# Optimization experiments

Hardware: AMD Instinct MI355X
Metric: run time of the kernel (lower is better)

## Reference

```python
import jax, jax.numpy as jnp
import numpy as np

B, T, N, C, H, K, L, E = 8, 16, 512, 64, 64, 3, 2, 16384


def setup_inputs() -> dict:
    key = jax.random.key(0)
    ks = jax.random.split(key, 8)
    x = jax.random.normal(ks[0], (B, T, N, C), jnp.float32)
    edge_index = jax.random.randint(ks[1], (2, E), 0, N, dtype=jnp.int64)
    edge_weight = jax.random.uniform(ks[2], (E,), jnp.float32)
    s = 0.05
    # per layer l, gate g in (z, r, h): K Chebyshev weight mats for x-conv and h-conv
    Wx = jax.random.normal(ks[3], (L, 3, K, C, H), jnp.float32) * s
    bx = jnp.zeros((L, 3, H), jnp.float32)
    Wh = jax.random.normal(ks[4], (L, 3, K, H, H), jnp.float32) * s
    bh = jnp.zeros((L, 3, H), jnp.float32)
    W1 = jax.random.normal(ks[5], (2 * H, H), jnp.float32) * s
    b1 = jnp.zeros((H,), jnp.float32)
    W2 = jax.random.normal(ks[6], (H, 1), jnp.float32) * s
    b2 = jnp.zeros((1,), jnp.float32)
    return dict(x=x, edge_weight=edge_weight, Wx=Wx, bx=bx, Wh=Wh, bh=bh,
                W1=W1, b1=b1, W2=W2, b2=b2, edge_index=edge_index)


def _cheb(t, W, b, src, dst, norm_w):
    # ChebConv with sym norm, lambda_max=2: L_hat = -D^{-1/2} A D^{-1/2} (zero diag)
    # t: [B, N, Cin], W: [K, Cin, H], b: [H]
    def Lx(u):
        msg = u[:, src, :] * norm_w[None, :, None]  # gather + scale per edge
        return jnp.zeros_like(u).at[:, dst, :].add(msg)  # scatter-add to targets
    out = jnp.einsum('bnc,ch->bnh', t, W[0])
    Tprev, Tcur = t, Lx(t)
    out = out + jnp.einsum('bnc,ch->bnh', Tcur, W[1])
    for k in range(2, W.shape[0]):
        Tnext = 2.0 * Lx(Tcur) - Tprev
        out = out + jnp.einsum('bnc,ch->bnh', Tnext, W[k])
        Tprev, Tcur = Tcur, Tnext
    return out + b


def _gru_cell(x_t, h, Wx_l, bx_l, Wh_l, bh_l, src, dst, norm_w):
    z = jax.nn.sigmoid(_cheb(x_t, Wx_l[0], bx_l[0], src, dst, norm_w)
                       + _cheb(h, Wh_l[0], bh_l[0], src, dst, norm_w))
    r = jax.nn.sigmoid(_cheb(x_t, Wx_l[1], bx_l[1], src, dst, norm_w)
                       + _cheb(h, Wh_l[1], bh_l[1], src, dst, norm_w))
    h_tilde = jnp.tanh(_cheb(x_t, Wx_l[2], bx_l[2], src, dst, norm_w)
                       + _cheb(h * r, Wh_l[2], bh_l[2], src, dst, norm_w))
    return z * h + (1.0 - z) * h_tilde


def reference(x, edge_weight, Wx, bx, Wh, bh, W1, b1, W2, b2, edge_index):
    n = x.shape[2]
    src, dst = edge_index[0], edge_index[1]
    deg = jnp.zeros((n,), x.dtype).at[src].add(edge_weight)
    dinv = jnp.where(deg > 0, jax.lax.rsqrt(jnp.maximum(deg, 1e-12)), 0.0)
    norm_w = -edge_weight * dinv[src] * dinv[dst]

    def step(h, x_t):
        for l in range(Wx.shape[0]):  # note: original passes the SAME x_t to every layer
            h = _gru_cell(x_t, h, Wx[l], bx[l], Wh[l], bh[l], src, dst, norm_w)
        return h, None

    h0 = jnp.zeros((x.shape[0], n, Wh.shape[-1]), x.dtype)
    h, _ = jax.lax.scan(step, h0, jnp.moveaxis(x, 1, 0))  # dropout is identity (eval)

    # all-pairs link predictor: cat(src_emb, tgt_emb) @ W1 split to avoid 2H concat
    hh = W1.shape[1]
    s_proj = h @ W1[:hh]   # [B, N, H]
    t_proj = h @ W1[hh:]   # [B, N, H]
    hid = jax.nn.relu(s_proj[:, :, None, :] + t_proj[:, None, :, :] + b1)  # [B,N,N,H]
    logits = jnp.einsum('bsth,ho->bsto', hid, W2)[..., 0] + b2[0]  # [B, N, N]
    return logits
```

## Files before the change

kernel.cpp:

```cpp
#include <hip/hip_runtime.h>

typedef unsigned short ushort;
typedef unsigned long long u64;
typedef __attribute__((ext_vector_type(8))) short short8;
typedef __attribute__((ext_vector_type(4))) float f32x4;

constexpr int Bn = 8, Tn = 16, Nn = 512, Cn = 64, Hn = 64, En = 16384, Ln = 2;
constexpr int NC = Nn * Cn;
constexpr int MROWS = Bn * Nn;

constexpr size_t OFF_DEG  = 0;
constexpr size_t OFF_DINV = 512;
constexpr size_t OFF_L1D  = 1024;
constexpr size_t OFF_L2D  = OFF_L1D + 262144;
constexpr size_t OFF_WZR  = OFF_L2D + 262144;
constexpr size_t OFF_WHT  = OFF_WZR + 2*384*128;
constexpr size_t OFF_BZR  = OFF_WHT + 2*384*64;
constexpr size_t OFF_BHT  = OFF_BZR + 256;
constexpr size_t OFF_W1C  = OFF_BHT + 128;
constexpr size_t OFF_T1X  = OFF_W1C + 8192;
constexpr size_t OFF_T2X  = OFF_T1X + (size_t)Bn*Tn*NC;
constexpr size_t OFF_H    = OFF_T2X + (size_t)Bn*Tn*NC;
constexpr size_t OFF_Z    = OFF_H   + (size_t)Bn*NC;
constexpr size_t OFF_HR   = OFF_Z   + (size_t)Bn*NC;
constexpr size_t OFF_SP   = OFF_HR  + (size_t)Bn*NC;
constexpr size_t OFF_TP   = OFF_SP  + (size_t)MROWS*Hn;
constexpr size_t OFF_LFH  = OFF_TP  + (size_t)MROWS*Hn;
constexpr size_t OFF_LFL  = OFF_LFH + 262144;
constexpr size_t OFF_HTH  = OFF_LFL + 262144;
constexpr size_t OFF_HTL  = OFF_HTH + 131072;
constexpr size_t OFF_HRTH = OFF_HTL + 131072;
constexpr size_t OFF_HRTL = OFF_HRTH + 131072;
constexpr size_t OFF_BAR  = OFF_HRTL + 131072;
constexpr size_t OFF_END  = OFF_BAR + 4096;

__device__ __forceinline__ ushort f2bf(float f) {
    unsigned u = __float_as_uint(f);
    u = u + 0x7FFF + ((u >> 16) & 1);
    return (ushort)(u >> 16);
}
__device__ __forceinline__ float bf2f(ushort h) {
    return __uint_as_float(((unsigned)h) << 16);
}
__device__ __forceinline__ int fragaddr(int m, int k) {
    return ((k >> 5) << 9) + (((k >> 3) & 3) << 7) + (m << 3) + (k & 7);
}

#define MFMA16(a, b, c) __builtin_amdgcn_mfma_f32_16x16x32_bf16((a), (b), (c), 0, 0, 0)

__global__ void k_deg(const float* __restrict__ w, const int* __restrict__ src,
                      float* __restrict__ deg) {
    int e = blockIdx.x * 256 + threadIdx.x;
    if (e < En) atomicAdd(&deg[src[e]], w[e]);
}

__global__ void k_dinv(const float* __restrict__ deg, float* __restrict__ dinv) {
    int n = blockIdx.x * 256 + threadIdx.x;
    if (n < Nn) {
        float d = deg[n];
        dinv[n] = d > 0.f ? rsqrtf(fmaxf(d, 1e-12f)) : 0.f;
    }
}

__global__ void k_nwdense(const float* __restrict__ w, const int* __restrict__ src,
                          const int* __restrict__ dst, const float* __restrict__ dinv,
                          float* __restrict__ L1d) {
    int e = blockIdx.x * 256 + threadIdx.x;
    if (e < En) {
        int s = src[e], d = dst[e];
        float nw = -w[e] * dinv[s] * dinv[d];
        atomicAdd(&L1d[d * Nn + s], nw);
    }
}

__global__ __launch_bounds__(1024) void k_l2(const float* __restrict__ A,
                                             float* __restrict__ C) {
    __shared__ float As[64][33];
    __shared__ float Bs[32][65];
    int t = threadIdx.x;
    int i0 = (blockIdx.x >> 3) * 64;
    int j0 = (blockIdx.x & 7) * 64;
    int tx = t & 31, ty = t >> 5;
    float acc[2][2] = {};
    int ar = t >> 4, ac = (t & 15) * 2;
    int br = t >> 5, bc = (t & 31) * 2;
    for (int kc = 0; kc < 512; kc += 32) {
        float2 a2 = *(const float2*)&A[(size_t)(i0 + ar) * 512 + kc + ac];
        float2 b2 = *(const float2*)&A[(size_t)(kc + br) * 512 + j0 + bc];
        As[ar][ac] = a2.x; As[ar][ac + 1] = a2.y;
        Bs[br][bc] = b2.x; Bs[br][bc + 1] = b2.y;
        __syncthreads();
#pragma unroll 8
        for (int kk = 0; kk < 32; kk++) {
            float a0 = As[ty * 2][kk], a1 = As[ty * 2 + 1][kk];
            float b0 = Bs[kk][tx * 2], b1 = Bs[kk][tx * 2 + 1];
            acc[0][0] += a0 * b0; acc[0][1] += a0 * b1;
            acc[1][0] += a1 * b0; acc[1][1] += a1 * b1;
        }
        __syncthreads();
    }
#pragma unroll
    for (int r = 0; r < 2; r++)
#pragma unroll
        for (int c = 0; c < 2; c++) {
            int i = i0 + ty * 2 + r, j = j0 + tx * 2 + c;
            C[(size_t)i * 512 + j] = 2.f * acc[r][c] - (i == j ? 1.f : 0.f);
        }
}

__global__ void k_lfrag(const float* __restrict__ L1, const float* __restrict__ L2,
                        ushort* __restrict__ AfH, ushort* __restrict__ AfL) {
    int idx = blockIdx.x * 256 + threadIdx.x;
    int j = idx & 7;
    int lane = (idx >> 3) & 63;
    int kc = (idx >> 9) & 15;
    int rb = (idx >> 13) & 31;
    int mat = idx >> 18;
    int row = rb * 16 + (lane & 15);
    int k = kc * 32 + (lane >> 4) * 8 + j;
    float v = (mat ? L2 : L1)[(size_t)row * 512 + k];
    ushort hi = f2bf(v);
    AfH[idx] = hi;
    AfL[idx] = f2bf(v - bf2f(hi));
}

__global__ void k_wfrag(const float* __restrict__ WzrC, const float* __restrict__ WhC,
                        ushort* __restrict__ WzFH, ushort* __restrict__ WzFL,
                        ushort* __restrict__ WhFH, ushort* __restrict__ WhFL) {
    int idx = blockIdx.x * 256 + threadIdx.x;
    if (idx < 98304) {
        int l = idx / 49152, off = idx % 49152;
        int tile = off >> 9, r = off & 511;
        int lane = r >> 3, j = r & 7;
        int ct = tile / 12, kc = tile % 12;
        int k = kc * 32 + (lane >> 4) * 8 + j;
        int n = ct * 16 + (lane & 15);
        float v = WzrC[(size_t)l * 49152 + k * 128 + n];
        ushort hi = f2bf(v);
        WzFH[idx] = hi;
        WzFL[idx] = f2bf(v - bf2f(hi));
    } else if (idx < 147456) {
        int t2 = idx - 98304;
        int l = t2 / 24576, off = t2 % 24576;
        int tile = off >> 9, r = off & 511;
        int lane = r >> 3, j = r & 7;
        int ct = tile / 12, kc = tile % 12;
        int k = kc * 32 + (lane >> 4) * 8 + j;
        int n = ct * 16 + (lane & 15);
        float v = WhC[(size_t)l * 24576 + k * 64 + n];
        ushort hi = f2bf(v);
        WhFH[t2] = hi;
        WhFL[t2] = f2bf(v - bf2f(hi));
    }
}

__global__ __launch_bounds__(256) void k_lxm(
        const ushort* __restrict__ AfH, const ushort* __restrict__ AfL,
        const float* __restrict__ in, float* __restrict__ o1, float* __restrict__ o2) {
    __shared__ ushort Bh[2][2176];
    __shared__ ushort Bl[2][2176];
    int slice = blockIdx.x >> 3;
    int rg = blockIdx.x & 7;
    const float* xs = in + (size_t)slice * NC;
    int tid = threadIdx.x;
    int lane = tid & 63, wav = tid >> 6;
    int quad = lane >> 4, l15 = lane & 15;
    int sn = tid & 63, skq = tid >> 6;
    int rt = rg * 4 + wav;
    size_t abA = ((size_t)rt * 16) * 512 + lane * 8;
    size_t abB = ((size_t)(32 + rt) * 16) * 512 + lane * 8;
    f32x4 accA[4], accB[4];
#pragma unroll
    for (int n = 0; n < 4; n++) {
        accA[n] = (f32x4){0.f, 0.f, 0.f, 0.f};
        accB[n] = (f32x4){0.f, 0.f, 0.f, 0.f};
    }
    {
        short8 hi8, lo8;
#pragma unroll
        for (int i = 0; i < 8; i++) {
            float v = xs[(size_t)(skq * 8 + i) * 64 + sn];
            ushort hv = f2bf(v);
            hi8[i] = (short)hv;
            lo8[i] = (short)f2bf(v - bf2f(hv));
        }
        *(short8*)&Bh[0][sn * 34 + skq * 8] = hi8;
        *(short8*)&Bl[0][sn * 34 + skq * 8] = lo8;
    }
    __syncthreads();
#pragma unroll
    for (int kc = 0; kc < 16; kc++) {
        const int cur = kc & 1;
        float sv[8];
        if (kc < 15) {
#pragma unroll
            for (int i = 0; i < 8; i++)
                sv[i] = xs[(size_t)((kc + 1) * 32 + skq * 8 + i) * 64 + sn];
        }
        size_t o = (size_t)kc * 512;
        short8 lah = *(const short8*)&AfH[abA + o];
        short8 lal = *(const short8*)&AfL[abA + o];
        short8 lbh = *(const short8*)&AfH[abB + o];
        short8 lbl = *(const short8*)&AfL[abB + o];
#pragma unroll
        for (int nt = 0; nt < 4; nt++) {
            short8 xh = *(const short8*)&Bh[cur][(nt * 16 + l15) * 34 + quad * 8];
            short8 xl = *(const short8*)&Bl[cur][(nt * 16 + l15) * 34 + quad * 8];
            accA[nt] = MFMA16(lah, xh, accA[nt]);
            accA[nt] = MFMA16(lah, xl, accA[nt]);
            accA[nt] = MFMA16(lal, xh, accA[nt]);
            accB[nt] = MFMA16(lbh, xh, accB[nt]);
            accB[nt] = MFMA16(lbh, xl, accB[nt]);
            accB[nt] = MFMA16(lbl, xh, accB[nt]);
        }
        if (kc < 15) {
            short8 hi8, lo8;
#pragma unroll
            for (int i = 0; i < 8; i++) {
                ushort hv = f2bf(sv[i]);
                hi8[i] = (short)hv;
                lo8[i] = (short)f2bf(sv[i] - bf2f(hv));
            }
            *(short8*)&Bh[cur ^ 1][sn * 34 + skq * 8] = hi8;
            *(short8*)&Bl[cur ^ 1][sn * 34 + skq * 8] = lo8;
        }
        __syncthreads();
    }
    float* os1 = o1 + (size_t)slice * NC;
    float* os2 = o2 + (size_t)slice * NC;
#pragma unroll
    for (int nt = 0; nt < 4; nt++)
#pragma unroll
        for (int reg = 0; reg < 4; reg++) {
            size_t row = (size_t)(rt * 16 + quad * 4 + reg);
            os1[row * 64 + nt * 16 + l15] = accA[nt][reg];
            os2[row * 64 + nt * 16 + l15] = accB[nt][reg];
        }
}

__global__ void k_repack(const float* __restrict__ Wx, const float* __restrict__ bx,
                         const float* __restrict__ Wh, const float* __restrict__ bh,
                         const float* __restrict__ W1,
                         float* __restrict__ WzrC, float* __restrict__ WhC,
                         float* __restrict__ bzr, float* __restrict__ bht,
                         float* __restrict__ W1cat) {
    int idx = blockIdx.x * 256 + threadIdx.x;
    if (idx < 98304) {
        int l = idx / 49152, r = idx % 49152;
        int k = r / 128, j = r % 128;
        int g = j >> 6, hh = j & 63;
        int kc, c; const float* s;
        if (k < 64)       { kc = 0; c = k; s = Wh; }
        else if (k < 256) { kc = (k - 64) >> 6; c = (k - 64) & 63; s = Wx; }
        else              { kc = 1 + ((k - 256) >> 6); c = (k - 256) & 63; s = Wh; }
        WzrC[idx] = s[((((size_t)(l*3 + g))*3 + kc)*64 + c)*64 + hh];
    } else if (idx < 147456) {
        int tI = idx - 98304;
        int l = tI / 24576, r = tI % 24576;
        int k = r / 64, hh = r % 64;
        int kc, c; const float* s;
        if (k < 64)       { kc = 0; c = k; s = Wh; }
        else if (k < 256) { kc = (k - 64) >> 6; c = (k - 64) & 63; s = Wx; }
        else              { kc = 1 + ((k - 256) >> 6); c = (k - 256) & 63; s = Wh; }
        WhC[tI] = s[((((size_t)(l*3 + 2))*3 + kc)*64 + c)*64 + hh];
    } else if (idx < 147712) {
        int tI = idx - 147456;
        int l = tI >> 7, j = tI & 127;
        int g = j >> 6, hh = j & 63;
        bzr[tI] = bh[(l*3 + g)*64 + hh] + bx[(l*3 + g)*64 + hh];
    } else if (idx < 147840) {
        int tI = idx - 147712;
        int l = tI >> 6, hh = tI & 63;
        bht[tI] = bh[(l*3 + 2)*64 + hh] + bx[(l*3 + 2)*64 + hh];
    } else if (idx < 156032) {
        int tI = idx - 147840;
        int c = tI >> 7, j = tI & 127;
        W1cat[tI] = (j < 64) ? W1[c*64 + j] : W1[(64 + c)*64 + (j - 64)];
    }
}


__device__ __forceinline__ void wait_flags(int* gflags, int epoch) {
    if (threadIdx.x < 64) {
        bool done = threadIdx.x >= 32;
        while (!__all(done)) {
            if (!done)
                done = __hip_atomic_load(&gflags[threadIdx.x * 16],
                                         __ATOMIC_RELAXED,
                                         __HIP_MEMORY_SCOPE_AGENT) >= epoch;
            if (!__all(done)) __builtin_amdgcn_s_sleep(1);
        }
    }
    __syncthreads();
}

__device__ __forceinline__ void arrive(int* gflags, int rowblk, int epoch) {
    asm volatile("s_waitcnt vmcnt(0)" ::: "memory");
    __syncthreads();
    if (threadIdx.x == 0)
        __hip_atomic_store(&gflags[rowblk * 16], epoch,
                           __ATOMIC_RELAXED, __HIP_MEMORY_SCOPE_AGENT);
}

__device__ __forceinline__ void store_T_pay(ushort* dstB, const float* S,
                                            int n0, int tid) {
    if (tid < 128) {
        int c = tid >> 1, half = tid & 1;
        short8 v;
#pragma unroll
        for (int j = 0; j < 8; j++)
            v[j] = (short)f2bf(S[(half * 8 + j) * 64 + c]);
        asm volatile("global_store_dwordx4 %0, %1, off sc0 sc1"
                     :: "v"(dstB + (size_t)c * 512 + n0 + half * 8), "v"(v)
                     : "memory");
    }
}

__device__ __forceinline__ void stage_xsegs(
        ushort* AH, ushort* AL, const float* __restrict__ x,
        const float* __restrict__ t1x, const float* __restrict__ t2x,
        size_t xoff, int tid) {
    int p = tid * 4;
    int m = p >> 6, kb = p & 63;
    int fa = fragaddr(m, kb);
    const float* srcs[3] = { x + xoff, t1x + xoff, t2x + xoff };
    const int sidx[3] = { 1, 2, 3 };
#pragma unroll
    for (int q = 0; q < 3; q++) {
        float4 v = *(const float4*)&srcs[q][(size_t)m * 64 + kb];
        float vv[4] = { v.x, v.y, v.z, v.w };
        int base = sidx[q] * 1024 + fa;
#pragma unroll
        for (int j = 0; j < 4; j++) {
            ushort hi = f2bf(vv[j]);
            AH[base + j] = hi;
            AL[base + j] = f2bf(vv[j] - bf2f(hi));
        }
    }
}

__device__ __forceinline__ void stage_h_lds(ushort* AH, ushort* AL,
                                            const float* hs, int tid) {
    int p = tid * 4;
    int m = p >> 6, kb = p & 63;
    int fa = fragaddr(m, kb);
#pragma unroll
    for (int j = 0; j < 4; j++) {
        float v = hs[m * 64 + kb + j];
        ushort hi = f2bf(v);
        AH[fa + j] = hi;
        AL[fa + j] = f2bf(v - bf2f(hi));
    }
}

__device__ __forceinline__ void phase_A16_p(
        ushort* AH, ushort* AL, const ushort* LAH, const ushort* LAL,
        const ushort* __restrict__ sTh, int tid) {
    int lane = tid & 63, wav = tid >> 6;
    int quad = lane >> 4, l15 = lane & 15;
    int ab1 = lane * 8;
    int ab2 = 8192 + lane * 8;
    size_t bb = (size_t)(wav * 16 + l15) * 512 + quad * 8;
    f32x4 p1a = {0.f,0.f,0.f,0.f}, p1c = p1a, p2a = p1a, p2c = p1a;
    short8 bh[16];
#pragma unroll
    for (int s = 0; s < 16; s++) {
        asm volatile("global_load_dwordx4 %0, %1, off sc0 sc1"
                     : "=v"(bh[s]) : "v"(sTh + bb + (size_t)s * 32) : "memory");
    }
    asm volatile("s_waitcnt vmcnt(0)" ::: "memory");
    __builtin_amdgcn_sched_barrier(0);
    short8 a1h[2], a1l[2], a2h[2], a2l[2];
#pragma unroll
    for (int s = 0; s < 2; s++) {
        int o = s * 512;
        a1h[s] = *(const short8*)&LAH[ab1 + o];
        a1l[s] = *(const short8*)&LAL[ab1 + o];
        a2h[s] = *(const short8*)&LAH[ab2 + o];
        a2l[s] = *(const short8*)&LAL[ab2 + o];
    }
#pragma unroll
    for (int kc = 0; kc < 16; kc++) {
        int sa = kc & 1;
        p1a = MFMA16(a1h[sa], bh[kc], p1a);
        p1c = MFMA16(a1l[sa], bh[kc], p1c);
        p2a = MFMA16(a2h[sa], bh[kc], p2a);
        p2c = MFMA16(a2l[sa], bh[kc], p2c);
        if (kc + 2 < 16) {
            int o = (kc + 2) * 512;
            a1h[sa] = *(const short8*)&LAH[ab1 + o];
            a1l[sa] = *(const short8*)&LAL[ab1 + o];
            a2h[sa] = *(const short8*)&LAH[ab2 + o];
            a2l[sa] = *(const short8*)&LAL[ab2 + o];
        }
    }
    int colA = wav * 16 + l15;
#pragma unroll
    for (int reg = 0; reg < 4; reg++) {
        int row = quad * 4 + reg;
        float u1 = p1a[reg] + p1c[reg];
        float u2 = p2a[reg] + p2c[reg];
        ushort h1 = f2bf(u1), h2 = f2bf(u2);
        int fa1 = 4096 + fragaddr(row, colA);
        int fa2 = 5120 + fragaddr(row, colA);
        AH[fa1] = h1; AL[fa1] = f2bf(u1 - bf2f(h1));
        AH[fa2] = h2; AL[fa2] = f2bf(u2 - bf2f(h2));
    }
}

__device__ __forceinline__ void phase_B1_pre(
        const ushort* AH, const ushort* AL,
        const ushort* __restrict__ WFH, const ushort* __restrict__ WFL,
        f32x4* q, int tid) {
    int lane = tid & 63, wav = tid >> 6;
    int quad = lane >> 4, l15 = lane & 15;
    int abase = quad * 128 + l15 * 8;
    size_t w0 = ((size_t)wav * 12) * 512 + lane * 8;
    size_t w1 = ((size_t)(4 + wav) * 12) * 512 + lane * 8;
    short8 ah[2], al[2], w0h[4], w0l[4], w1h[4], w1l[4];
#pragma unroll
    for (int s = 0; s < 2; s++) {
        ah[s] = *(const short8*)&AH[abase + s * 512];
        al[s] = *(const short8*)&AL[abase + s * 512];
    }
#pragma unroll
    for (int s = 0; s < 4; s++) {
        size_t o = (size_t)s * 512;
        w0h[s] = *(const short8*)&WFH[w0 + o];
        w0l[s] = *(const short8*)&WFL[w0 + o];
        w1h[s] = *(const short8*)&WFH[w1 + o];
        w1l[s] = *(const short8*)&WFL[w1 + o];
    }
#pragma unroll
    for (int kt = 0; kt < 8; kt++) {
        int sa = kt & 1, sw = kt & 3;
        q[0] = MFMA16(ah[sa], w0h[sw], q[0]);
        q[1] = MFMA16(ah[sa], w0l[sw], q[1]);
        q[2] = MFMA16(al[sa], w0h[sw], q[2]);
        q[3] = MFMA16(ah[sa], w1h[sw], q[3]);
        q[4] = MFMA16(ah[sa], w1l[sw], q[4]);
        q[5] = MFMA16(al[sa], w1h[sw], q[5]);
        if (kt + 2 < 8) {
            ah[sa] = *(const short8*)&AH[abase + (kt + 2) * 512];
            al[sa] = *(const short8*)&AL[abase + (kt + 2) * 512];
        }
        if (kt + 4 < 8) {
            size_t o = (size_t)(kt + 4) * 512;
            w0h[sw] = *(const short8*)&WFH[w0 + o];
            w0l[sw] = *(const short8*)&WFL[w0 + o];
            w1h[sw] = *(const short8*)&WFH[w1 + o];
            w1l[sw] = *(const short8*)&WFL[w1 + o];
        }
    }
}

__device__ __forceinline__ void phase_B1_post(
        const ushort* AH, const ushort* AL,
        const ushort* __restrict__ WFH, const ushort* __restrict__ WFL,
        f32x4* q, float* PRED, int tid) {
    int lane = tid & 63, wav = tid >> 6;
    int quad = lane >> 4, l15 = lane & 15;
    int abase = quad * 128 + l15 * 8;
    size_t w0 = ((size_t)wav * 12) * 512 + lane * 8;
    size_t w1 = ((size_t)(4 + wav) * 12) * 512 + lane * 8;
    short8 ah[4], al[4], w0h[4], w0l[4], w1h[4], w1l[4];
#pragma unroll
    for (int s = 0; s < 4; s++) {
        int o = (8 + s) * 512;
        ah[s] = *(const short8*)&AH[abase + o];
        al[s] = *(const short8*)&AL[abase + o];
        size_t wo = (size_t)(8 + s) * 512;
        w0h[s] = *(const short8*)&WFH[w0 + wo];
        w0l[s] = *(const short8*)&WFL[w0 + wo];
        w1h[s] = *(const short8*)&WFH[w1 + wo];
        w1l[s] = *(const short8*)&WFL[w1 + wo];
    }
#pragma unroll
    for (int kt = 0; kt < 4; kt++) {
        q[0] = MFMA16(ah[kt], w0h[kt], q[0]);
        q[1] = MFMA16(ah[kt], w0l[kt], q[1]);
        q[2] = MFMA16(al[kt], w0h[kt], q[2]);
        q[3] = MFMA16(ah[kt], w1h[kt], q[3]);
        q[4] = MFMA16(ah[kt], w1l[kt], q[4]);
        q[5] = MFMA16(al[kt], w1h[kt], q[5]);
    }
#pragma unroll
    for (int reg = 0; reg < 4; reg++) {
        int row = quad * 4 + reg;
        PRED[row * 128 + wav * 16 + l15] = q[0][reg] + q[1][reg] + q[2][reg];
        PRED[row * 128 + 64 + wav * 16 + l15] = q[3][reg] + q[4][reg] + q[5][reg];
    }
}

__device__ __forceinline__ void phase_B2_pre(
        const ushort* AH, const ushort* AL,
        const ushort* __restrict__ WFH, const ushort* __restrict__ WFL,
        f32x4* q, int tid) {
    int lane = tid & 63, wav = tid >> 6;
    int quad = lane >> 4, l15 = lane & 15;
    int abase = quad * 128 + l15 * 8;
    size_t w0 = ((size_t)wav * 12) * 512 + lane * 8;
    short8 ah[2], al[2], wh[4], wl[4];
#pragma unroll
    for (int s = 0; s < 2; s++) {
        ah[s] = *(const short8*)&AH[abase + s * 512];
        al[s] = *(const short8*)&AL[abase + s * 512];
    }
#pragma unroll
    for (int s = 0; s < 4; s++) {
        wh[s] = *(const short8*)&WFH[w0 + (size_t)s * 512];
        wl[s] = *(const short8*)&WFL[w0 + (size_t)s * 512];
    }
#pragma unroll
    for (int kt = 0; kt < 8; kt++) {
        int sa = kt & 1, sw = kt & 3;
        q[0] = MFMA16(ah[sa], wh[sw], q[0]);
        q[1] = MFMA16(ah[sa], wl[sw], q[1]);
        q[2] = MFMA16(al[sa], wh[sw], q[2]);
        if (kt + 2 < 8) {
            ah[sa] = *(const short8*)&AH[abase + (kt + 2) * 512];
            al[sa] = *(const short8*)&AL[abase + (kt + 2) * 512];
        }
        if (kt + 4 < 8) {
            size_t o = (size_t)(kt + 4) * 512;
            wh[sw] = *(const short8*)&WFH[w0 + o];
            wl[sw] = *(const short8*)&WFL[w0 + o];
        }
    }
}

__device__ __forceinline__ void phase_B2_post(
        const ushort* AH, const ushort* AL,
        const ushort* __restrict__ WFH, const ushort* __restrict__ WFL,
        f32x4* q, float* PRED, int tid) {
    int lane = tid & 63, wav = tid >> 6;
    int quad = lane >> 4, l15 = lane & 15;
    int abase = quad * 128 + l15 * 8;
    size_t w0 = ((size_t)wav * 12) * 512 + lane * 8;
    short8 ah[4], al[4], wh[4], wl[4];
#pragma unroll
    for (int s = 0; s < 4; s++) {
        int o = (8 + s) * 512;
        ah[s] = *(const short8*)&AH[abase + o];
        al[s] = *(const short8*)&AL[abase + o];
        size_t wo = (size_t)(8 + s) * 512;
        wh[s] = *(const short8*)&WFH[w0 + wo];
        wl[s] = *(const short8*)&WFL[w0 + wo];
    }
#pragma unroll
    for (int kt = 0; kt < 4; kt++) {
        q[0] = MFMA16(ah[kt], wh[kt], q[0]);
        q[1] = MFMA16(ah[kt], wl[kt], q[1]);
        q[2] = MFMA16(al[kt], wh[kt], q[2]);
    }
#pragma unroll
    for (int reg = 0; reg < 4; reg++)
        PRED[(quad * 4 + reg) * 64 + wav * 16 + l15] = q[0][reg] + q[1][reg] + q[2][reg];
}

__global__ __launch_bounds__(256) void k_recur(
        const float* __restrict__ x, const float* __restrict__ t1x,
        const float* __restrict__ t2x,
        const ushort* __restrict__ AfH, const ushort* __restrict__ AfL,
        const ushort* __restrict__ WzFH, const ushort* __restrict__ WzFL,
        const ushort* __restrict__ WhFH, const ushort* __restrict__ WhFL,
        const float* __restrict__ bzr, const float* __restrict__ bht,
        float* __restrict__ h, ushort* __restrict__ hTh,
        ushort* __restrict__ hrTh, int* __restrict__ bar) {
    __shared__ __attribute__((aligned(16))) ushort AH[6144];
    __shared__ __attribute__((aligned(16))) ushort AL[6144];
    __shared__ __attribute__((aligned(16))) float  PRED[2048];
    __shared__ __attribute__((aligned(16))) float  HS[1024];
    __shared__ __attribute__((aligned(16))) float  ZS[1024];
    __shared__ __attribute__((aligned(16))) float  HRS[1024];
    __shared__ __attribute__((aligned(16))) ushort LAH[16384];
    __shared__ __attribute__((aligned(16))) ushort LAL[16384];
    int tid = threadIdx.x;
    int b = blockIdx.x & 7;
    int rowblk = blockIdx.x >> 3;
    int n0 = rowblk * 16;
    int* gflags = bar + b * 512;

    for (int i = tid; i < 1024; i += 256) {
        *(short8*)&LAH[i * 8] = *(const short8*)&AfH[(size_t)rowblk * 8192 + i * 8];
        *(short8*)&LAL[i * 8] = *(const short8*)&AfL[(size_t)rowblk * 8192 + i * 8];
        *(short8*)&LAH[8192 + i * 8] = *(const short8*)&AfH[(size_t)(32 + rowblk) * 8192 + i * 8];
        *(short8*)&LAL[8192 + i * 8] = *(const short8*)&AfL[(size_t)(32 + rowblk) * 8192 + i * 8];
    }
    for (int i = tid; i < 1024; i += 256) HS[i] = 0.f;
    __syncthreads();

    ushort* hThB = hTh + (size_t)b * 32768;
    ushort* hrThB = hrTh + (size_t)b * 32768;
    int ep = 0;
#pragma unroll 1
    for (int t = 0; t < Tn; t++) {
        size_t xoff = ((size_t)(b * Tn + t) * Nn + n0) * 64;
        stage_xsegs(AH, AL, x, t1x, t2x, xoff, tid);
#pragma unroll 1
        for (int l = 0; l < Ln; l++) {
            const ushort* WzH = WzFH + (size_t)l * 49152;
            const ushort* WzL = WzFL + (size_t)l * 49152;
            const ushort* WtH = WhFH + (size_t)l * 24576;
            const ushort* WtL = WhFL + (size_t)l * 24576;
            const float* bz = bzr + l * 128;
            const float* bt = bht + l * 64;
            stage_h_lds(AH, AL, HS, tid);
            __syncthreads();
            f32x4 q[6];
#pragma unroll
            for (int i = 0; i < 6; i++) q[i] = (f32x4){0.f,0.f,0.f,0.f};
            phase_B1_pre(AH, AL, WzH, WzL, q, tid);
            wait_flags(gflags, ep);
            phase_A16_p(AH, AL, LAH, LAL, hThB, tid);
            __syncthreads();
            phase_B1_post(AH, AL, WzH, WzL, q, PRED, tid);
            __syncthreads();
            for (int i = tid; i < 2048; i += 256) {
                int r = i >> 7, c = i & 127;
                float v = PRED[i] + bz[c];
                float s = 1.f / (1.f + __expf(-v));
                if (c < 64) {
                    ZS[r * 64 + c] = s;
                } else {
                    int c2 = c - 64;
                    HRS[r * 64 + c2] = HS[r * 64 + c2] * s;
                }
            }
            __syncthreads();
            store_T_pay(hrThB, HRS, n0, tid);
            arrive(gflags, rowblk, ep + 1);
            ep++;
            stage_h_lds(AH, AL, HRS, tid);
            __syncthreads();
            f32x4 r3[3];
#pragma unroll
            for (int i = 0; i < 3; i++) r3[i] = (f32x4){0.f,0.f,0.f,0.f};
            phase_B2_pre(AH, AL, WtH, WtL, r3, tid);
            wait_flags(gflags, ep);
            phase_A16_p(AH, AL, LAH, LAL, hrThB, tid);
            __syncthreads();
            phase_B2_post(AH, AL, WtH, WtL, r3, PRED, tid);
            __syncthreads();
            for (int i = tid; i < 1024; i += 256) {
                int c = i & 63;
                float v = PRED[i] + bt[c];
                float av = fabsf(v);
                float e2 = __expf(-2.f * av);
                float m = (1.f - e2) / (1.f + e2);
                float htv = v < 0.f ? -m : m;
                float zz = ZS[i], hold = HS[i];
                float hn = zz * hold + (1.f - zz) * htv;
                HS[i] = hn;
                if (t == Tn - 1 && l == Ln - 1)
                    h[((size_t)(b * Nn + n0 + (i >> 6))) * 64 + c] = hn;
            }
            __syncthreads();
            store_T_pay(hThB, HS, n0, tid);
            arrive(gflags, rowblk, ep + 1);
            ep++;
        }
    }
}

__global__ __launch_bounds__(256) void k_proj(
        const float* __restrict__ h, const float* __restrict__ W1cat,
        const float* __restrict__ b1,
        float* __restrict__ sproj, float* __restrict__ tproj) {
    __shared__ float As[16][33];
    __shared__ float Ws[16 * 128];
    int tid = threadIdx.x;
    int row0 = blockIdx.x * 32;
    const float* hp = h + (size_t)row0 * 64;
    float acc[2][8] = {};
    int tx = tid & 15, ty = tid >> 4;
    int lr = tid >> 3;
    int lk = (tid & 7) * 2;
    int wk = tid >> 4;
    int wc = (tid & 15) * 8;
    for (int kt = 0; kt < 4; kt++) {
        int c0 = kt * 16;
        float2 a2 = *(const float2*)&hp[lr * 64 + c0 + lk];
        const float4* wsrc = (const float4*)&W1cat[(size_t)(kt * 16 + wk) * 128 + wc];
        float4 w0 = wsrc[0], w1 = wsrc[1];
        As[lk][lr] = a2.x;
        As[lk + 1][lr] = a2.y;
        *(float4*)&Ws[wk * 128 + wc] = w0;
        *(float4*)&Ws[wk * 128 + wc + 4] = w1;
        __syncthreads();
#pragma unroll
        for (int kk = 0; kk < 16; kk++) {
            float a0 = As[kk][ty * 2 + 0];
            float a1 = As[kk][ty * 2 + 1];
            float4 p0 = *(const float4*)&Ws[kk * 128 + tx * 8];
            float4 p1 = *(const float4*)&Ws[kk * 128 + tx * 8 + 4];
            float w[8] = { p0.x, p0.y, p0.z, p0.w, p1.x, p1.y, p1.z, p1.w };
#pragma unroll
            for (int cc = 0; cc < 8; cc++) {
                acc[0][cc] += a0 * w[cc];
                acc[1][cc] += a1 * w[cc];
            }
        }
        __syncthreads();
    }
#pragma unroll
    for (int rr = 0; rr < 2; rr++) {
        int row = row0 + ty * 2 + rr;
#pragma unroll
        for (int cc = 0; cc < 8; cc++) {
            int col = tx * 8 + cc;
            float v = acc[rr][cc];
            if (col < 64) sproj[(size_t)row * 64 + col] = v + b1[col];
            else tproj[(size_t)row * 64 + (col - 64)] = v;
        }
    }
}

__global__ __launch_bounds__(256) void k_logits(
        const float* __restrict__ sproj, const float* __restrict__ tproj,
        const float* __restrict__ W2, const float* __restrict__ b2,
        float* __restrict__ out) {
    __shared__ float sp[32 * 64];
    __shared__ float tp[64 * 65];
    __shared__ float w2s[64];
    int tid = threadIdx.x;
    int bb = blockIdx.x >> 7;
    int st = (blockIdx.x >> 3) & 15;
    int tt = blockIdx.x & 7;
    const float* spg = sproj + ((size_t)bb * Nn + st * 32) * 64;
    const float* tpg = tproj + ((size_t)bb * Nn + tt * 64) * 64;
    for (int i = tid; i < 2048; i += 256) sp[i] = spg[i];
    for (int i = tid; i < 4096; i += 256) {
        int tl = i >> 6, hh = i & 63;
        tp[tl * 65 + hh] = tpg[i];
    }
    if (tid < 64) w2s[tid] = W2[tid];
    __syncthreads();
    float bias = *b2;
    int tl = tid & 63, sg = tid >> 6;
    for (int si = 0; si < 8; si++) {
        int s = sg * 8 + si;
        float acc = bias;
#pragma unroll 8
        for (int hh = 0; hh < 64; hh++) {
            float v = sp[s * 64 + hh] + tp[tl * 65 + hh];
            acc += fmaxf(v, 0.f) * w2s[hh];
        }
        out[(size_t)bb * Nn * Nn + (size_t)(st * 32 + s) * Nn + tt * 64 + tl] = acc;
    }
}

extern "C" void kernel_launch(void* const* d_in, const int* in_sizes, int n_in,
                              void* d_out, int out_size, void* d_ws, size_t ws_size,
                              hipStream_t stream) {
    const float* x  = (const float*)d_in[0];
    const float* ew = (const float*)d_in[1];
    const float* Wx = (const float*)d_in[2];
    const float* bx = (const float*)d_in[3];
    const float* Wh = (const float*)d_in[4];
    const float* bh = (const float*)d_in[5];
    const float* W1 = (const float*)d_in[6];
    const float* b1 = (const float*)d_in[7];
    const float* W2 = (const float*)d_in[8];
    const float* b2 = (const float*)d_in[9];
    const int* ei   = (const int*)d_in[10];
    const int* esrc = ei;
    const int* edst = ei + En;

    float* ws = (float*)d_ws;
    float* deg   = ws + OFF_DEG;
    float* dinv  = ws + OFF_DINV;
    float* L1d   = ws + OFF_L1D;
    float* L2d   = ws + OFF_L2D;
    float* WzrC  = ws + OFF_WZR;
    float* WhC   = ws + OFF_WHT;
    float* bzr   = ws + OFF_BZR;
    float* bht   = ws + OFF_BHT;
    float* W1cat = ws + OFF_W1C;
    float* T1x   = ws + OFF_T1X;
    float* T2x   = ws + OFF_T2X;
    float* h     = ws + OFF_H;
    float* sproj = ws + OFF_SP;
    float* tproj = ws + OFF_TP;
    ushort* AfH  = (ushort*)(ws + OFF_LFH);
    ushort* AfL  = (ushort*)(ws + OFF_LFL);
    ushort* hTh  = (ushort*)(ws + OFF_HTH);
    ushort* hrTh = (ushort*)(ws + OFF_HRTH);
    int* bar     = (int*)(ws + OFF_BAR);
    ushort* WzFH = (ushort*)(ws + OFF_SP);
    ushort* WzFL = WzFH + 98304;
    ushort* WhFH = WzFL + 98304;
    ushort* WhFL = WhFH + 49152;
    float* out   = (float*)d_out;

    hipMemsetAsync(deg, 0, 512 * sizeof(float), stream);
    hipMemsetAsync(L1d, 0, (size_t)Nn * Nn * sizeof(float), stream);
    hipMemsetAsync(h, 0, (size_t)Bn * NC * sizeof(float), stream);
    hipMemsetAsync(hTh, 0, 262144 * sizeof(ushort), stream);
    hipMemsetAsync(bar, 0, 4096 * sizeof(int), stream);

    k_deg<<<64, 256, 0, stream>>>(ew, esrc, deg);
    k_dinv<<<2, 256, 0, stream>>>(deg, dinv);
    k_nwdense<<<64, 256, 0, stream>>>(ew, esrc, edst, dinv, L1d);
    k_l2<<<64, 1024, 0, stream>>>(L1d, L2d);
    k_lfrag<<<2048, 256, 0, stream>>>(L1d, L2d, AfH, AfL);
    k_repack<<<(156032 + 255) / 256, 256, 0, stream>>>(Wx, bx, Wh, bh, W1,
                                                       WzrC, WhC, bzr, bht, W1cat);
    k_wfrag<<<(147456 + 255) / 256, 256, 0, stream>>>(WzrC, WhC, WzFH, WzFL, WhFH, WhFL);

    k_lxm<<<1024, 256, 0, stream>>>(AfH, AfL, x, T1x, T2x);

    k_recur<<<256, 256, 0, stream>>>(x, T1x, T2x, AfH, AfL, WzFH, WzFL,
                                     WhFH, WhFL, bzr, bht, h, hTh, hrTh, bar);

    k_proj<<<128, 256, 0, stream>>>(h, W1cat, b1, sproj, tproj);
    k_logits<<<Bn * 16 * 8, 256, 0, stream>>>(sproj, tproj, W2, b2, out);
}
```

Baseline: 681.3 us.

## Process two batches per block in recurrent kernel to halve grid

The persistent recurrent GRU kernel now handles two batch elements (b and b+4) per block for the same row block. The grid drops from 256 to 128 blocks, and the L-fragment LDS tile is shared between the two batches. Each phase is interleaved across the two batches so one batch's flag wait can overlap with the other's MFMA work, and both flags are signalled together. In exchange, the work per block doubles and LDS use grows, which limits occupancy to one block per CU, with fewer CUs in use.

```diff
diff --git a/kernel.cpp b/kernel.cpp
--- a/kernel.cpp
+++ b/kernel.cpp
@@ -294,11 +294,14 @@
     __syncthreads();
 }
 
-__device__ __forceinline__ void arrive(int* gflags, int rowblk, int epoch) {
+__device__ __forceinline__ void arrive2(int* gfA, int* gfB, int rowblk, int epoch) {
     asm volatile("s_waitcnt vmcnt(0)" ::: "memory");
     __syncthreads();
     if (threadIdx.x == 0)
-        __hip_atomic_store(&gflags[rowblk * 16], epoch,
+        __hip_atomic_store(&gfA[rowblk * 16], epoch,
+                           __ATOMIC_RELAXED, __HIP_MEMORY_SCOPE_AGENT);
+    else if (threadIdx.x == 64)
+        __hip_atomic_store(&gfB[rowblk * 16], epoch,
                            __ATOMIC_RELAXED, __HIP_MEMORY_SCOPE_AGENT);
 }
 
@@ -558,7 +561,7 @@
         PRED[(quad * 4 + reg) * 64 + wav * 16 + l15] = q[0][reg] + q[1][reg] + q[2][reg];
 }
 
-__global__ __launch_bounds__(256) void k_recur(
+__global__ __launch_bounds__(256, 1) void k_recur(
         const float* __restrict__ x, const float* __restrict__ t1x,
         const float* __restrict__ t2x,
         const ushort* __restrict__ AfH, const ushort* __restrict__ AfL,
@@ -567,19 +570,19 @@
         const float* __restrict__ bzr, const float* __restrict__ bht,
         float* __restrict__ h, ushort* __restrict__ hTh,
         ushort* __restrict__ hrTh, int* __restrict__ bar) {
-    __shared__ __attribute__((aligned(16))) ushort AH[6144];
-    __shared__ __attribute__((aligned(16))) ushort AL[6144];
-    __shared__ __attribute__((aligned(16))) float  PRED[2048];
-    __shared__ __attribute__((aligned(16))) float  HS[1024];
-    __shared__ __attribute__((aligned(16))) float  ZS[1024];
-    __shared__ __attribute__((aligned(16))) float  HRS[1024];
-    __shared__ __attribute__((aligned(16))) ushort LAH[16384];
-    __shared__ __attribute__((aligned(16))) ushort LAL[16384];
+    __shared__ __attribute__((aligned(16))) ushort AH0[6144], AL0[6144];
+    __shared__ __attribute__((aligned(16))) ushort AH1[6144], AL1[6144];
+    __shared__ __attribute__((aligned(16))) float  PRED0[2048], PRED1[2048];
+    __shared__ __attribute__((aligned(16))) float  HS0[1024], ZS0[1024], HRS0[1024];
+    __shared__ __attribute__((aligned(16))) float  HS1[1024], ZS1[1024], HRS1[1024];
+    __shared__ __attribute__((aligned(16))) ushort LAH[16384], LAL[16384];
     int tid = threadIdx.x;
-    int b = blockIdx.x & 7;
-    int rowblk = blockIdx.x >> 3;
+    int g = blockIdx.x >> 5;
+    int bA = g, bB = g + 4;
+    int rowblk = blockIdx.x & 31;
     int n0 = rowblk * 16;
-    int* gflags = bar + b * 512;
+    int* gfA = bar + bA * 512;
+    int* gfB = bar + bB * 512;
 
     for (int i = tid; i < 1024; i += 256) {
         *(short8*)&LAH[i * 8] = *(const short8*)&AfH[(size_t)rowblk * 8192 + i * 8];
@@ -587,16 +590,20 @@
         *(short8*)&LAH[8192 + i * 8] = *(const short8*)&AfH[(size_t)(32 + rowblk) * 8192 + i * 8];
         *(short8*)&LAL[8192 + i * 8] = *(const short8*)&AfL[(size_t)(32 + rowblk) * 8192 + i * 8];
     }
-    for (int i = tid; i < 1024; i += 256) HS[i] = 0.f;
+    for (int i = tid; i < 1024; i += 256) { HS0[i] = 0.f; HS1[i] = 0.f; }
     __syncthreads();
 
-    ushort* hThB = hTh + (size_t)b * 32768;
-    ushort* hrThB = hrTh + (size_t)b * 32768;
+    ushort* hThA  = hTh  + (size_t)bA * 32768;
+    ushort* hrThA = hrTh + (size_t)bA * 32768;
+    ushort* hThB_ = hTh  + (size_t)bB * 32768;
+    ushort* hrThB_= hrTh + (size_t)bB * 32768;
     int ep = 0;
 #pragma unroll 1
     for (int t = 0; t < Tn; t++) {
-        size_t xoff = ((size_t)(b * Tn + t) * Nn + n0) * 64;
-        stage_xsegs(AH, AL, x, t1x, t2x, xoff, tid);
+        size_t xoffA = ((size_t)(bA * Tn + t) * Nn + n0) * 64;
+        size_t xoffB = ((size_t)(bB * Tn + t) * Nn + n0) * 64;
+        stage_xsegs(AH0, AL0, x, t1x, t2x, xoffA, tid);
+        stage_xsegs(AH1, AL1, x, t1x, t2x, xoffB, tid);
 #pragma unroll 1
         for (int l = 0; l < Ln; l++) {
             const ushort* WzH = WzFH + (size_t)l * 49152;
@@ -605,59 +612,87 @@
             const ushort* WtL = WhFL + (size_t)l * 24576;
             const float* bz = bzr + l * 128;
             const float* bt = bht + l * 64;
-            stage_h_lds(AH, AL, HS, tid);
+            stage_h_lds(AH0, AL0, HS0, tid);
+            stage_h_lds(AH1, AL1, HS1, tid);
             __syncthreads();
-            f32x4 q[6];
-#pragma unroll
-            for (int i = 0; i < 6; i++) q[i] = (f32x4){0.f,0.f,0.f,0.f};
-            phase_B1_pre(AH, AL, WzH, WzL, q, tid);
-            wait_flags(gflags, ep);
-            phase_A16_p(AH, AL, LAH, LAL, hThB, tid);
+            f32x4 qA[6], qB[6];
+#pragma unroll
+            for (int i = 0; i < 6; i++) { qA[i] = (f32x4){0.f,0.f,0.f,0.f}; qB[i] = qA[i]; }
+            phase_B1_pre(AH0, AL0, WzH, WzL, qA, tid);
+            phase_B1_pre(AH1, AL1, WzH, WzL, qB, tid);
+            wait_flags(gfA, ep);
+            phase_A16_p(AH0, AL0, LAH, LAL, hThA, tid);
+            wait_flags(gfB, ep);
+            phase_A16_p(AH1, AL1, LAH, LAL, hThB_, tid);
             __syncthreads();
-            phase_B1_post(AH, AL, WzH, WzL, q, PRED, tid);
+            phase_B1_post(AH0, AL0, WzH, WzL, qA, PRED0, tid);
+            phase_B1_post(AH1, AL1, WzH, WzL, qB, PRED1, tid);
             __syncthreads();
             for (int i = tid; i < 2048; i += 256) {
                 int r = i >> 7, c = i & 127;
-                float v = PRED[i] + bz[c];
+                float v = PRED0[i] + bz[c];
                 float s = 1.f / (1.f + __expf(-v));
-                if (c < 64) {
-                    ZS[r * 64 + c] = s;
-                } else {
-                    int c2 = c - 64;
-                    HRS[r * 64 + c2] = HS[r * 64 + c2] * s;
-                }
+                if (c < 64) ZS0[r * 64 + c] = s;
+                else { int c2 = c - 64; HRS0[r * 64 + c2] = HS0[r * 64 + c2] * s; }
+            }
+            for (int i = tid; i < 2048; i += 256) {
+                int r = i >> 7, c = i & 127;
+                float v = PRED1[i] + bz[c];
+                float s = 1.f / (1.f + __expf(-v));
+                if (c < 64) ZS1[r * 64 + c] = s;
+                else { int c2 = c - 64; HRS1[r * 64 + c2] = HS1[r * 64 + c2] * s; }
             }
             __syncthreads();
-            store_T_pay(hrThB, HRS, n0, tid);
-            arrive(gflags, rowblk, ep + 1);
+            store_T_pay(hrThA, HRS0, n0, tid);
+            store_T_pay(hrThB_, HRS1, n0, tid);
+            arrive2(gfA, gfB, rowblk, ep + 1);
             ep++;
-            stage_h_lds(AH, AL, HRS, tid);
+            stage_h_lds(AH0, AL0, HRS0, tid);
+            stage_h_lds(AH1, AL1, HRS1, tid);
             __syncthreads();
-            f32x4 r3[3];
-#pragma unroll
-            for (int i = 0; i < 3; i++) r3[i] = (f32x4){0.f,0.f,0.f,0.f};
-            phase_B2_pre(AH, AL, WtH, WtL, r3, tid);
-            wait_flags(gflags, ep);
-            phase_A16_p(AH, AL, LAH, LAL, hrThB, tid);
+            f32x4 rA[3], rB[3];
+#pragma unroll
+            for (int i = 0; i < 3; i++) { rA[i] = (f32x4){0.f,0.f,0.f,0.f}; rB[i] = rA[i]; }
+            phase_B2_pre(AH0, AL0, WtH, WtL, rA, tid);
+            phase_B2_pre(AH1, AL1, WtH, WtL, rB, tid);
+            wait_flags(gfA, ep);
+            phase_A16_p(AH0, AL0, LAH, LAL, hrThA, tid);
+            wait_flags(gfB, ep);
+            phase_A16_p(AH1, AL1, LAH, LAL, hrThB_, tid);
             __syncthreads();
-            phase_B2_post(AH, AL, WtH, WtL, r3, PRED, tid);
+            phase_B2_post(AH0, AL0, WtH, WtL, rA, PRED0, tid);
+            phase_B2_post(AH1, AL1, WtH, WtL, rB, PRED1, tid);
             __syncthreads();
             for (int i = tid; i < 1024; i += 256) {
                 int c = i & 63;
-                float v = PRED[i] + bt[c];
+                float v = PRED0[i] + bt[c];
                 float av = fabsf(v);
                 float e2 = __expf(-2.f * av);
                 float m = (1.f - e2) / (1.f + e2);
                 float htv = v < 0.f ? -m : m;
-                float zz = ZS[i], hold = HS[i];
+                float zz = ZS0[i], hold = HS0[i];
                 float hn = zz * hold + (1.f - zz) * htv;
-                HS[i] = hn;
+                HS0[i] = hn;
                 if (t == Tn - 1 && l == Ln - 1)
-                    h[((size_t)(b * Nn + n0 + (i >> 6))) * 64 + c] = hn;
+                    h[((size_t)(bA * Nn + n0 + (i >> 6))) * 64 + c] = hn;
+            }
+            for (int i = tid; i < 1024; i += 256) {
+                int c = i & 63;
+                float v = PRED1[i] + bt[c];
+                float av = fabsf(v);
+                float e2 = __expf(-2.f * av);
+                float m = (1.f - e2) / (1.f + e2);
+                float htv = v < 0.f ? -m : m;
+                float zz = ZS1[i], hold = HS1[i];
+                float hn = zz * hold + (1.f - zz) * htv;
+                HS1[i] = hn;
+                if (t == Tn - 1 && l == Ln - 1)
+                    h[((size_t)(bB * Nn + n0 + (i >> 6))) * 64 + c] = hn;
             }
             __syncthreads();
-            store_T_pay(hThB, HS, n0, tid);
-            arrive(gflags, rowblk, ep + 1);
+            store_T_pay(hThA, HS0, n0, tid);
+            store_T_pay(hThB_, HS1, n0, tid);
+            arrive2(gfA, gfB, rowblk, ep + 1);
             ep++;
         }
     }
@@ -810,7 +845,7 @@
 
     k_lxm<<<1024, 256, 0, stream>>>(AfH, AfL, x, T1x, T2x);
 
-    k_recur<<<256, 256, 0, stream>>>(x, T1x, T2x, AfH, AfL, WzFH, WzFL,
+    k_recur<<<128, 256, 0, stream>>>(x, T1x, T2x, AfH, AfL, WzFH, WzFL,
                                      WhFH, WhFL, bzr, bht, h, hTh, hrTh, bar);
 
     k_proj<<<128, 256, 0, stream>>>(h, W1cat, b1, sproj, tproj);
```

New measurement: 1.019 ms. +49.5%, slower.
